# Kernel optimization log

Hardware: AMD Instinct MI355X
Metric: run time of the kernel (lower is better)

The kernel has to match this reference:

```python
import jax, jax.numpy as jnp
import numpy as np

B, S, D, C, WD, I = 8, 14, 2048, 20, 300, 1024  # batch, imgSize, imgFeatureDim, classNum, wordFeatureDim, intermediaDim


def setup_inputs() -> dict:
    key = jax.random.key(0)
    ks = jax.random.split(key, 8)
    s = 0.02
    return {
        "imgFeaturemap": jax.random.normal(ks[0], (B, S, S, D), jnp.float32),
        "wordFeatures": jax.random.normal(ks[1], (C, WD), jnp.float32),
        "W1": jax.random.normal(ks[2], (I, D), jnp.float32) * s,   # fc1, no bias
        "W2": jax.random.normal(ks[3], (I, WD), jnp.float32) * s,  # fc2, no bias
        "W3": jax.random.normal(ks[4], (I, I), jnp.float32) * s,   # fc3
        "b3": jax.random.normal(ks[5], (I,), jnp.float32) * s,
        "W4": jax.random.normal(ks[6], (1, I), jnp.float32) * s,   # fc4
        "b4": jax.random.normal(ks[7], (1,), jnp.float32) * s,
    }


def reference(imgFeaturemap, wordFeatures, W1, W2, W3, b3, W4, b4):
    b, s, _, d = imgFeaturemap.shape
    c = wordFeatures.shape[0]
    n = b * s * s  # number of spatial locations across batch

    h_img = imgFeaturemap.reshape(n, d) @ W1.T          # [N, I]
    h_word = wordFeatures @ W2.T                         # [C, I]
    # broadcasted elementwise product + tanh (original materializes via repeat)
    t = jnp.tanh(h_img[:, None, :] * h_word[None, :, :])  # [N, C, I]
    feat = t @ W3.T + b3                                  # [N, C, I]
    coef = (feat @ W4.T)[..., 0] + b4[0]                  # [N, C]
    # softmax over spatial positions per (batch, class)
    coef = jax.nn.softmax(coef.reshape(b, s * s, c), axis=1).reshape(b, s, s, c)
    # weighted feature map and class-wise pooled semantic features
    fmwc = imgFeaturemap[:, :, :, None, :] * coef[..., None]  # [B, S, S, C, D]
    semanticFeature = fmwc.sum(axis=(1, 2))                    # [B, C, D]
    return semanticFeature, fmwc, coef
```

## Files before the change

kernel.cpp:

```cpp
#include <hip/hip_runtime.h>

typedef __attribute__((ext_vector_type(4))) float float4_t;
typedef __attribute__((ext_vector_type(8))) short short8_t;
typedef __attribute__((ext_vector_type(4))) unsigned short ushort4_t;

#define B_ 8
#define S_ 14
#define P_ 196
#define N_ 1568
#define D_ 2048
#define C_ 20
#define WD_ 300
#define I_ 1024
#define PS_ 14
#define LROW 72

__device__ __forceinline__ unsigned short f2bf(float f) {
    unsigned u = __builtin_bit_cast(unsigned, f);
    u += 0x7FFFu + ((u >> 16) & 1u);
    return (unsigned short)(u >> 16);
}

__global__ __launch_bounds__(256) void cvt_prep_kernel(const float* __restrict__ img,
                                                       const float* __restrict__ W1,
                                                       unsigned short* __restrict__ Xb,
                                                       unsigned short* __restrict__ W1b,
                                                       const float* __restrict__ wf,
                                                       const float* __restrict__ W2,
                                                       const float* __restrict__ W3,
                                                       const float* __restrict__ b3,
                                                       const float* __restrict__ W4,
                                                       const float* __restrict__ b4,
                                                       float* __restrict__ hw,
                                                       float* __restrict__ we,
                                                       float* __restrict__ bias) {
    int bid = blockIdx.x, tid = threadIdx.x;
    if (bid < 5184) {
        const float* src;
        unsigned short* dst;
        int i4;
        if (bid < 3136) { i4 = bid * 256 + tid; src = img; dst = Xb; }
        else            { i4 = (bid - 3136) * 256 + tid; src = W1; dst = W1b; }
        float4_t v = ((const float4_t*)src)[i4];
        ushort4_t o;
        o.x = f2bf(v.x); o.y = f2bf(v.y); o.z = f2bf(v.z); o.w = f2bf(v.w);
        ((ushort4_t*)dst)[i4] = o;
        return;
    }
    int pb = bid - 5184;
    if (pb < 80) {
        int idx = pb * 256 + tid;
        int c = idx >> 10, i = idx & 1023;
        const float* wr  = wf + c * WD_;
        const float* w2r = W2 + i * WD_;
        float s = 0.f;
        #pragma unroll 4
        for (int k = 0; k < WD_; k++) s += wr[k] * w2r[k];
        hw[idx] = s;
    } else if (pb < 96) {
        __shared__ float red[256];
        int blk = pb - 80;
        int i0 = blk * 64;
        int q = tid >> 6, col = tid & 63;
        float s = 0.f;
        #pragma unroll 4
        for (int j = q * 256; j < q * 256 + 256; j++)
            s += W4[j] * W3[j * I_ + i0 + col];
        red[tid] = s;
        __syncthreads();
        if (tid < 64)
            we[i0 + tid] = red[tid] + red[tid + 64] + red[tid + 128] + red[tid + 192];
    } else {
        __shared__ float r[256];
        float s = 0.f;
        for (int j = tid; j < I_; j += 256) s += b3[j] * W4[j];
        r[tid] = s;
        __syncthreads();
        for (int o = 128; o > 0; o >>= 1) {
            if (tid < o) r[tid] += r[tid + o];
            __syncthreads();
        }
        if (tid == 0) bias[0] = r[0] + b4[0];
    }
}

__global__ __launch_bounds__(256) void gemm_himg_kernel(const unsigned short* __restrict__ Xb,
                                                        const unsigned short* __restrict__ W1b,
                                                        float* __restrict__ H) {
    __shared__ unsigned short lds[160 * LROW];
    int tid = threadIdx.x;
    int wave = tid >> 6, lane = tid & 63;
    int m0 = (blockIdx.x >> 3) * 32;
    int n0 = (blockIdx.x & 7) * 128;

    int arow = tid >> 3, ak16 = tid & 7;
    const unsigned short* gA = Xb + (size_t)(m0 + arow) * D_ + ak16 * 8;
    unsigned short* lA = &lds[arow * LROW + ak16 * 8];
    const unsigned short* gB[4];
    unsigned short* lB[4];
    #pragma unroll
    for (int j = 0; j < 4; j++) {
        int idx = tid + 256 * j;
        int brow = idx >> 3, bk16 = idx & 7;
        gB[j] = W1b + (size_t)(n0 + brow) * D_ + bk16 * 8;
        lB[j] = &lds[(32 + brow) * LROW + bk16 * 8];
    }

    int ra = lane & 15, kq = (lane >> 4) * 8;
    const unsigned short* Af = &lds[ra * LROW + kq];
    const unsigned short* Bf = &lds[(32 + wave * 32 + ra) * LROW + kq];

    float4_t acc[2][2] = {};
    short8_t sA = *(const short8_t*)(gA);
    short8_t sB0 = *(const short8_t*)(gB[0]);
    short8_t sB1 = *(const short8_t*)(gB[1]);
    short8_t sB2 = *(const short8_t*)(gB[2]);
    short8_t sB3 = *(const short8_t*)(gB[3]);

    for (int t = 0; t < 32; t++) {
        *(short8_t*)lA = sA;
        *(short8_t*)lB[0] = sB0;
        *(short8_t*)lB[1] = sB1;
        *(short8_t*)lB[2] = sB2;
        *(short8_t*)lB[3] = sB3;
        __syncthreads();

        if (t < 31) {
            int ko = (t + 1) * 64;
            sA  = *(const short8_t*)(gA + ko);
            sB0 = *(const short8_t*)(gB[0] + ko);
            sB1 = *(const short8_t*)(gB[1] + ko);
            sB2 = *(const short8_t*)(gB[2] + ko);
            sB3 = *(const short8_t*)(gB[3] + ko);
        }

        #pragma unroll
        for (int ks = 0; ks < 2; ks++) {
            short8_t a0 = *(const short8_t*)(Af + ks * 32);
            short8_t a1 = *(const short8_t*)(Af + 16 * LROW + ks * 32);
            short8_t b0 = *(const short8_t*)(Bf + ks * 32);
            short8_t b1 = *(const short8_t*)(Bf + 16 * LROW + ks * 32);
            acc[0][0] = __builtin_amdgcn_mfma_f32_16x16x32_bf16(a0, b0, acc[0][0], 0, 0, 0);
            acc[0][1] = __builtin_amdgcn_mfma_f32_16x16x32_bf16(a0, b1, acc[0][1], 0, 0, 0);
            acc[1][0] = __builtin_amdgcn_mfma_f32_16x16x32_bf16(a1, b0, acc[1][0], 0, 0, 0);
            acc[1][1] = __builtin_amdgcn_mfma_f32_16x16x32_bf16(a1, b1, acc[1][1], 0, 0, 0);
        }
        __syncthreads();
    }

    int col = lane & 15, rq = (lane >> 4) * 4;
    #pragma unroll
    for (int mt = 0; mt < 2; mt++) {
        #pragma unroll
        for (int nt = 0; nt < 2; nt++) {
            float4_t v = acc[mt][nt];
            int rbase = m0 + mt * 16 + rq;
            int cidx = n0 + wave * 32 + nt * 16 + col;
            H[(rbase + 0) * I_ + cidx] = v.x;
            H[(rbase + 1) * I_ + cidx] = v.y;
            H[(rbase + 2) * I_ + cidx] = v.z;
            H[(rbase + 3) * I_ + cidx] = v.w;
        }
    }
}

__global__ __launch_bounds__(256) void logits_kernel(const float* __restrict__ H,
                                                     const float* __restrict__ hw,
                                                     const float* __restrict__ we,
                                                     const float* __restrict__ bias,
                                                     float* __restrict__ lg) {
    __shared__ float sh[4][I_];
    __shared__ float sw[I_];
    int n0 = blockIdx.x * 4, tid = threadIdx.x;
    #pragma unroll
    for (int t = 0; t < 4; t++) {
        int idx = tid + 256 * t;
        sw[idx] = we[idx];
        #pragma unroll
        for (int nn = 0; nn < 4; nn++)
            sh[nn][idx] = H[(size_t)(n0 + nn) * I_ + idx];
    }
    __syncthreads();
    int wv = tid >> 6, lane = tid & 63;
    float bz = bias[0];
    for (int j = 0; j < 5; j++) {
        int c = j * 4 + wv;
        const float* hwc = hw + c * I_;
        float a0 = 0.f, a1 = 0.f, a2 = 0.f, a3 = 0.f;
        #pragma unroll 2
        for (int i = lane; i < I_; i += 64) {
            float hv = hwc[i], wvv = sw[i];
            float x0 = sh[0][i] * hv;
            float x1 = sh[1][i] * hv;
            float x2 = sh[2][i] * hv;
            float x3 = sh[3][i] * hv;
            float t0 = 1.f - __fdividef(2.f, __expf(2.f * x0) + 1.f);
            float t1 = 1.f - __fdividef(2.f, __expf(2.f * x1) + 1.f);
            float t2 = 1.f - __fdividef(2.f, __expf(2.f * x2) + 1.f);
            float t3 = 1.f - __fdividef(2.f, __expf(2.f * x3) + 1.f);
            a0 += t0 * wvv; a1 += t1 * wvv; a2 += t2 * wvv; a3 += t3 * wvv;
        }
        #pragma unroll
        for (int o = 32; o > 0; o >>= 1) {
            a0 += __shfl_down(a0, o);
            a1 += __shfl_down(a1, o);
            a2 += __shfl_down(a2, o);
            a3 += __shfl_down(a3, o);
        }
        if (lane == 0) {
            lg[(n0 + 0) * C_ + c] = a0 + bz;
            lg[(n0 + 1) * C_ + c] = a1 + bz;
            lg[(n0 + 2) * C_ + c] = a2 + bz;
            lg[(n0 + 3) * C_ + c] = a3 + bz;
        }
    }
}

__global__ __launch_bounds__(256) void softmax_kernel(const float* __restrict__ lg,
                                                      float* __restrict__ coef) {
    __shared__ float r[4];
    __shared__ float bval;
    int bx = blockIdx.x;
    int b = bx / C_, c = bx % C_;
    int tid = threadIdx.x, wv = tid >> 6, lane = tid & 63;
    float v = (tid < P_) ? lg[(b * P_ + tid) * C_ + c] : -3.0e38f;
    float m = v;
    #pragma unroll
    for (int o = 32; o > 0; o >>= 1) m = fmaxf(m, __shfl_down(m, o));
    if (lane == 0) r[wv] = m;
    __syncthreads();
    if (tid == 0) bval = fmaxf(fmaxf(r[0], r[1]), fmaxf(r[2], r[3]));
    __syncthreads();
    float mx = bval;
    float e = (tid < P_) ? __expf(v - mx) : 0.f;
    float s = e;
    #pragma unroll
    for (int o = 32; o > 0; o >>= 1) s += __shfl_down(s, o);
    __syncthreads();
    if (lane == 0) r[wv] = s;
    __syncthreads();
    if (tid == 0) bval = r[0] + r[1] + r[2] + r[3];
    __syncthreads();
    if (tid < P_) coef[(b * P_ + tid) * C_ + c] = e / bval;
}

__global__ __launch_bounds__(256) void fmwc_kernel(const float* __restrict__ img,
                                                   const float* __restrict__ coef,
                                                   float* __restrict__ fm) {
    __shared__ float sc[C_];
    int bp = blockIdx.x, tid = threadIdx.x;
    if (tid < C_) sc[tid] = coef[bp * C_ + tid];
    __syncthreads();
    const float4_t* ir = (const float4_t*)(img + (size_t)bp * D_);
    float4_t v0 = ir[tid], v1 = ir[tid + 256];
    float4_t* ob = (float4_t*)(fm + (size_t)bp * C_ * D_);
    #pragma unroll
    for (int c = 0; c < C_; c++) {
        float s = sc[c];
        ob[c * 512 + tid] = v0 * s;
        ob[c * 512 + tid + 256] = v1 * s;
    }
}

__global__ __launch_bounds__(256) void semantic_part_kernel(const float* __restrict__ img,
                                                            const float* __restrict__ coef,
                                                            float* __restrict__ part) {
    __shared__ float sc[PS_ * C_];
    int bx = blockIdx.x;
    int ps = bx >> 4;
    int b = (bx >> 1) & 7;
    int ch = bx & 1;
    int tid = threadIdx.x;
    for (int q = tid; q < PS_ * C_; q += 256)
        sc[q] = coef[(b * P_ + ps * PS_) * C_ + q];
    __syncthreads();
    const float4_t* base = (const float4_t*)(img + (size_t)(b * P_ + ps * PS_) * D_ + ch * 1024) + tid;
    float4_t acc[C_];
    #pragma unroll
    for (int c = 0; c < C_; c++) acc[c] = (float4_t){0.f, 0.f, 0.f, 0.f};
    for (int pp = 0; pp < PS_; pp++) {
        float4_t v = base[pp * 512];
        #pragma unroll
        for (int c = 0; c < C_; c++) acc[c] += v * sc[pp * C_ + c];
    }
    float* pb = part + ((size_t)(ps * B_ + b) * C_) * D_ + ch * 1024 + tid * 4;
    #pragma unroll
    for (int c = 0; c < C_; c++) *(float4_t*)(pb + c * D_) = acc[c];
}

__global__ __launch_bounds__(256) void semantic_reduce_kernel(const float* __restrict__ part,
                                                              float* __restrict__ sem) {
    int idx = blockIdx.x * 256 + threadIdx.x;
    const float4_t* p4 = (const float4_t*)part;
    float4_t s = {0.f, 0.f, 0.f, 0.f};
    #pragma unroll
    for (int ps = 0; ps < PS_; ps++) s += p4[(size_t)ps * 81920 + idx];
    ((float4_t*)sem)[idx] = s;
}

extern "C" void kernel_launch(void* const* d_in, const int* in_sizes, int n_in,
                              void* d_out, int out_size, void* d_ws, size_t ws_size,
                              hipStream_t stream) {
    const float* img = (const float*)d_in[0];
    const float* wf  = (const float*)d_in[1];
    const float* W1  = (const float*)d_in[2];
    const float* W2  = (const float*)d_in[3];
    const float* W3  = (const float*)d_in[4];
    const float* b3  = (const float*)d_in[5];
    const float* W4  = (const float*)d_in[6];
    const float* b4  = (const float*)d_in[7];

    float* out  = (float*)d_out;
    float* sem  = out;
    float* fm   = out + (size_t)B_ * C_ * D_;
    float* coef = fm + (size_t)N_ * C_ * D_;

    char* ws = (char*)d_ws;
    unsigned short* Xb  = (unsigned short*)ws;
    unsigned short* W1b = (unsigned short*)(ws + 6422528);
    float* H    = (float*)(ws + 10616832);
    float* hw   = (float*)(ws + 17039360);
    float* we   = (float*)(ws + 17121280);
    float* bias = (float*)(ws + 17125376);
    float* lg   = (float*)(ws + 17125632);
    float* part = (float*)(ws + 17251072);

    cvt_prep_kernel<<<5281, 256, 0, stream>>>(img, W1, Xb, W1b, wf, W2, W3, b3, W4, b4, hw, we, bias);
    gemm_himg_kernel<<<392, 256, 0, stream>>>(Xb, W1b, H);
    logits_kernel<<<N_ / 4, 256, 0, stream>>>(H, hw, we, bias, lg);
    softmax_kernel<<<B_ * C_, 256, 0, stream>>>(lg, coef);
    semantic_part_kernel<<<PS_ * B_ * 2, 256, 0, stream>>>(img, coef, part);
    semantic_reduce_kernel<<<320, 256, 0, stream>>>(part, sem);
    fmwc_kernel<<<N_, 256, 0, stream>>>(img, coef, fm);
}
```

Before: 403.5 us.

## Restructure logits kernel per row and merge semantic-part with fmwc launch

The logits kernel now runs one block per spatial location, with each wave handling five classes, instead of four locations per block looping over classes. This gives 1568 blocks rather than 392, trading more hw reads from L2 for more parallelism. The semantic partial-sum and fmwc broadcast kernels are merged into one launch using block-index branching. This removes a launch and lets the small reduction overlap with the large fmwc write stream.

```diff
diff --git a/kernel.cpp b/kernel.cpp
--- a/kernel.cpp
+++ b/kernel.cpp
@@ -169,50 +169,55 @@
                                                      const float* __restrict__ we,
                                                      const float* __restrict__ bias,
                                                      float* __restrict__ lg) {
-    __shared__ float sh[4][I_];
+    __shared__ float sh[I_];
     __shared__ float sw[I_];
-    int n0 = blockIdx.x * 4, tid = threadIdx.x;
+    int n = blockIdx.x, tid = threadIdx.x;
     #pragma unroll
     for (int t = 0; t < 4; t++) {
         int idx = tid + 256 * t;
         sw[idx] = we[idx];
-        #pragma unroll
-        for (int nn = 0; nn < 4; nn++)
-            sh[nn][idx] = H[(size_t)(n0 + nn) * I_ + idx];
+        sh[idx] = H[(size_t)n * I_ + idx];
     }
     __syncthreads();
     int wv = tid >> 6, lane = tid & 63;
     float bz = bias[0];
-    for (int j = 0; j < 5; j++) {
-        int c = j * 4 + wv;
-        const float* hwc = hw + c * I_;
-        float a0 = 0.f, a1 = 0.f, a2 = 0.f, a3 = 0.f;
-        #pragma unroll 2
-        for (int i = lane; i < I_; i += 64) {
-            float hv = hwc[i], wvv = sw[i];
-            float x0 = sh[0][i] * hv;
-            float x1 = sh[1][i] * hv;
-            float x2 = sh[2][i] * hv;
-            float x3 = sh[3][i] * hv;
-            float t0 = 1.f - __fdividef(2.f, __expf(2.f * x0) + 1.f);
-            float t1 = 1.f - __fdividef(2.f, __expf(2.f * x1) + 1.f);
-            float t2 = 1.f - __fdividef(2.f, __expf(2.f * x2) + 1.f);
-            float t3 = 1.f - __fdividef(2.f, __expf(2.f * x3) + 1.f);
-            a0 += t0 * wvv; a1 += t1 * wvv; a2 += t2 * wvv; a3 += t3 * wvv;
-        }
-        #pragma unroll
-        for (int o = 32; o > 0; o >>= 1) {
-            a0 += __shfl_down(a0, o);
-            a1 += __shfl_down(a1, o);
-            a2 += __shfl_down(a2, o);
-            a3 += __shfl_down(a3, o);
-        }
-        if (lane == 0) {
-            lg[(n0 + 0) * C_ + c] = a0 + bz;
-            lg[(n0 + 1) * C_ + c] = a1 + bz;
-            lg[(n0 + 2) * C_ + c] = a2 + bz;
-            lg[(n0 + 3) * C_ + c] = a3 + bz;
-        }
+
+    int c0 = wv, c1 = 4 + wv, c2 = 8 + wv, c3 = 12 + wv, c4 = 16 + wv;
+    const float* h0 = hw + c0 * I_;
+    const float* h1 = hw + c1 * I_;
+    const float* h2 = hw + c2 * I_;
+    const float* h3 = hw + c3 * I_;
+    const float* h4 = hw + c4 * I_;
+    float a0 = 0.f, a1 = 0.f, a2 = 0.f, a3 = 0.f, a4 = 0.f;
+    #pragma unroll 2
+    for (int i = lane; i < I_; i += 64) {
+        float s = sh[i], wvv = sw[i];
+        float x0 = s * h0[i];
+        float x1 = s * h1[i];
+        float x2 = s * h2[i];
+        float x3 = s * h3[i];
+        float x4 = s * h4[i];
+        float t0 = 1.f - __fdividef(2.f, __expf(2.f * x0) + 1.f);
+        float t1 = 1.f - __fdividef(2.f, __expf(2.f * x1) + 1.f);
+        float t2 = 1.f - __fdividef(2.f, __expf(2.f * x2) + 1.f);
+        float t3 = 1.f - __fdividef(2.f, __expf(2.f * x3) + 1.f);
+        float t4 = 1.f - __fdividef(2.f, __expf(2.f * x4) + 1.f);
+        a0 += t0 * wvv; a1 += t1 * wvv; a2 += t2 * wvv; a3 += t3 * wvv; a4 += t4 * wvv;
+    }
+    #pragma unroll
+    for (int o = 32; o > 0; o >>= 1) {
+        a0 += __shfl_down(a0, o);
+        a1 += __shfl_down(a1, o);
+        a2 += __shfl_down(a2, o);
+        a3 += __shfl_down(a3, o);
+        a4 += __shfl_down(a4, o);
+    }
+    if (lane == 0) {
+        lg[n * C_ + c0] = a0 + bz;
+        lg[n * C_ + c1] = a1 + bz;
+        lg[n * C_ + c2] = a2 + bz;
+        lg[n * C_ + c3] = a3 + bz;
+        lg[n * C_ + c4] = a4 + bz;
     }
 }
 
@@ -244,48 +249,46 @@
     if (tid < P_) coef[(b * P_ + tid) * C_ + c] = e / bval;
 }
 
-__global__ __launch_bounds__(256) void fmwc_kernel(const float* __restrict__ img,
-                                                   const float* __restrict__ coef,
-                                                   float* __restrict__ fm) {
-    __shared__ float sc[C_];
-    int bp = blockIdx.x, tid = threadIdx.x;
-    if (tid < C_) sc[tid] = coef[bp * C_ + tid];
-    __syncthreads();
-    const float4_t* ir = (const float4_t*)(img + (size_t)bp * D_);
-    float4_t v0 = ir[tid], v1 = ir[tid + 256];
-    float4_t* ob = (float4_t*)(fm + (size_t)bp * C_ * D_);
-    #pragma unroll
-    for (int c = 0; c < C_; c++) {
-        float s = sc[c];
-        ob[c * 512 + tid] = v0 * s;
-        ob[c * 512 + tid + 256] = v1 * s;
-    }
-}
-
-__global__ __launch_bounds__(256) void semantic_part_kernel(const float* __restrict__ img,
-                                                            const float* __restrict__ coef,
-                                                            float* __restrict__ part) {
-    __shared__ float sc[PS_ * C_];
-    int bx = blockIdx.x;
-    int ps = bx >> 4;
-    int b = (bx >> 1) & 7;
-    int ch = bx & 1;
-    int tid = threadIdx.x;
-    for (int q = tid; q < PS_ * C_; q += 256)
-        sc[q] = coef[(b * P_ + ps * PS_) * C_ + q];
-    __syncthreads();
-    const float4_t* base = (const float4_t*)(img + (size_t)(b * P_ + ps * PS_) * D_ + ch * 1024) + tid;
-    float4_t acc[C_];
-    #pragma unroll
-    for (int c = 0; c < C_; c++) acc[c] = (float4_t){0.f, 0.f, 0.f, 0.f};
-    for (int pp = 0; pp < PS_; pp++) {
-        float4_t v = base[pp * 512];
-        #pragma unroll
-        for (int c = 0; c < C_; c++) acc[c] += v * sc[pp * C_ + c];
-    }
-    float* pb = part + ((size_t)(ps * B_ + b) * C_) * D_ + ch * 1024 + tid * 4;
-    #pragma unroll
-    for (int c = 0; c < C_; c++) *(float4_t*)(pb + c * D_) = acc[c];
+__global__ __launch_bounds__(256) void part_fmwc_kernel(const float* __restrict__ img,
+                                                        const float* __restrict__ coef,
+                                                        float* __restrict__ part,
+                                                        float* __restrict__ fm) {
+    int bid = blockIdx.x, tid = threadIdx.x;
+    if (bid < 224) {
+        __shared__ float sc[PS_ * C_];
+        int ps = bid >> 4;
+        int b = (bid >> 1) & 7;
+        int ch = bid & 1;
+        for (int q = tid; q < PS_ * C_; q += 256)
+            sc[q] = coef[(b * P_ + ps * PS_) * C_ + q];
+        __syncthreads();
+        const float4_t* base = (const float4_t*)(img + (size_t)(b * P_ + ps * PS_) * D_ + ch * 1024) + tid;
+        float4_t acc[C_];
+        #pragma unroll
+        for (int c = 0; c < C_; c++) acc[c] = (float4_t){0.f, 0.f, 0.f, 0.f};
+        for (int pp = 0; pp < PS_; pp++) {
+            float4_t v = base[pp * 512];
+            #pragma unroll
+            for (int c = 0; c < C_; c++) acc[c] += v * sc[pp * C_ + c];
+        }
+        float* pb = part + ((size_t)(ps * B_ + b) * C_) * D_ + ch * 1024 + tid * 4;
+        #pragma unroll
+        for (int c = 0; c < C_; c++) *(float4_t*)(pb + c * D_) = acc[c];
+    } else {
+        __shared__ float sc2[C_];
+        int bp = bid - 224;
+        if (tid < C_) sc2[tid] = coef[bp * C_ + tid];
+        __syncthreads();
+        const float4_t* ir = (const float4_t*)(img + (size_t)bp * D_);
+        float4_t v0 = ir[tid], v1 = ir[tid + 256];
+        float4_t* ob = (float4_t*)(fm + (size_t)bp * C_ * D_);
+        #pragma unroll
+        for (int c = 0; c < C_; c++) {
+            float s = sc2[c];
+            ob[c * 512 + tid] = v0 * s;
+            ob[c * 512 + tid + 256] = v1 * s;
+        }
+    }
 }
 
 __global__ __launch_bounds__(256) void semantic_reduce_kernel(const float* __restrict__ part,
@@ -327,9 +330,8 @@
 
     cvt_prep_kernel<<<5281, 256, 0, stream>>>(img, W1, Xb, W1b, wf, W2, W3, b3, W4, b4, hw, we, bias);
     gemm_himg_kernel<<<392, 256, 0, stream>>>(Xb, W1b, H);
-    logits_kernel<<<N_ / 4, 256, 0, stream>>>(H, hw, we, bias, lg);
+    logits_kernel<<<N_, 256, 0, stream>>>(H, hw, we, bias, lg);
     softmax_kernel<<<B_ * C_, 256, 0, stream>>>(lg, coef);
-    semantic_part_kernel<<<PS_ * B_ * 2, 256, 0, stream>>>(img, coef, part);
+    part_fmwc_kernel<<<224 + N_, 256, 0, stream>>>(img, coef, part, fm);
     semantic_reduce_kernel<<<320, 256, 0, stream>>>(part, sem);
-    fmwc_kernel<<<N_, 256, 0, stream>>>(img, coef, fm);
-}
+}
```

Result: faster. 388.7 us (-3.7%).
